# Optimization experiments

Hardware: AMD Instinct MI355X
Metric: run time of the kernel (lower is better)

Reference implementation:

```python
import jax, jax.numpy as jnp
import numpy as np
from jax import lax

B, L, D, H, OM = 16, 512, 2048, 512, 5


def _lstm(seq, wih, whh, bih, bhh):
    # seq: [T, B, F]; PyTorch gate order i, f, g, o
    Hh = whh.shape[1]
    Bb = seq.shape[1]
    def step(carry, xt):
        h, c = carry
        g = xt @ wih.T + h @ whh.T + bih + bhh
        i, f, gg, o = jnp.split(g, 4, axis=-1)
        c = jax.nn.sigmoid(f) * c + jax.nn.sigmoid(i) * jnp.tanh(gg)
        h = jax.nn.sigmoid(o) * jnp.tanh(c)
        return (h, c), h
    z = jnp.zeros((Bb, Hh), seq.dtype)
    _, hs = lax.scan(step, (z, z), seq)
    return hs  # [T, B, Hh]


def setup_inputs() -> dict:
    key = jax.random.key(0)
    ks = jax.random.split(key, 17)
    s = 0.02
    f32 = jnp.float32
    inp = {
        "x": jax.random.normal(ks[0], (B, L, D), f32),
        "wb": jax.random.normal(ks[1], (H, D, OM), f32) * s,
        "bb": jax.random.normal(ks[2], (H,), f32) * s,
        "wa": jax.random.normal(ks[3], (H, D, OM), f32) * s,
        "ba": jax.random.normal(ks[4], (H,), f32) * s,
        "wr": jax.random.normal(ks[5], (H, D, 2 * OM), f32) * s,
        "br": jax.random.normal(ks[6], (H,), f32) * s,
        "wih_f": jax.random.normal(ks[7], (4 * H, H + 1), f32) * s,
        "whh_f": jax.random.normal(ks[8], (4 * H, H), f32) * s,
        "bih_f": jax.random.normal(ks[9], (4 * H,), f32) * s,
        "bhh_f": jax.random.normal(ks[10], (4 * H,), f32) * s,
        "wih_r": jax.random.normal(ks[11], (4 * H, H + 1), f32) * s,
        "whh_r": jax.random.normal(ks[12], (4 * H, H), f32) * s,
        "bih_r": jax.random.normal(ks[13], (4 * H,), f32) * s,
        "bhh_r": jax.random.normal(ks[14], (4 * H,), f32) * s,
        "wfc": jax.random.normal(ks[15], (1, 2 * H), f32) * s,
        "bfc": jax.random.normal(ks[16], (1,), f32) * s,
    }
    return inp


def reference(x, wb, bb, wa, ba, wr, br, wih_f, whh_f, bih_f, bhh_f,
              wih_r, whh_r, bih_r, bhh_r, wfc, bfc):
    om = OM
    xc = jnp.transpose(x, (0, 2, 1))  # [B, D, L]
    conv = lambda w, b: lax.conv_general_dilated(
        xc, w, (1,), 'VALID', dimension_numbers=('NCH', 'OIH', 'NCH')) + b[None, :, None]
    cb = conv(wb, bb)  # [B, H, L-om+1]
    ca = conv(wa, ba)  # [B, H, L-om+1]
    cr = conv(wr, br)  # [B, H, L-2om+1]
    T = x.shape[1] - 2 * om  # number of centers c in [om, L-om)
    d_before = cb[:, :, 0:T]          # window [c-om, c) == conv output c-om
    d_after = ca[:, :, om:om + T]     # window [c, c+om) == conv output c
    vts_d = jnp.sum(d_before * d_after, axis=1, keepdims=True)  # [B, 1, T]
    vts_r = cr[:, :, 0:T]             # full window; pool over length-1 is identity
    vts_seq = jnp.concatenate([vts_r, vts_d], axis=1)  # [B, H+1, T]
    seq = jnp.transpose(vts_seq, (2, 0, 1))  # [T, B, H+1]
    hs_f = _lstm(seq, wih_f, whh_f, bih_f, bhh_f)
    hs_r = _lstm(seq[::-1], wih_r, whh_r, bih_r, bhh_r)[::-1]
    h = jnp.concatenate([hs_f, hs_r], axis=-1)  # [T, B, 2H]
    logits = jnp.einsum('tbh,h->tb', h, wfc[0]) + bfc[0]
    return jax.nn.sigmoid(jnp.transpose(logits))  # [B, T]
```

## Files before the change

### kernel.cpp

```cpp
#include <hip/hip_runtime.h>
#include <hip/hip_bf16.h>

typedef short v8s __attribute__((ext_vector_type(8)));
typedef float v4f __attribute__((ext_vector_type(4)));
typedef unsigned int u32;
typedef unsigned int u32x4 __attribute__((ext_vector_type(4)));
typedef unsigned short u16;
typedef unsigned long long u64;

__device__ __forceinline__ u16 f2bf(float f) {
    union { float f; u32 u; } x; x.f = f;
    u32 r = x.u + 0x7fffu + ((x.u >> 16) & 1u);
    return (u16)(r >> 16);
}
__device__ __forceinline__ float bf2f(u16 s) {
    union { u32 u; float f; } x; x.u = ((u32)s) << 16;
    return x.f;
}
__device__ __forceinline__ float sigmoidf_(float x) { return 1.f / (1.f + __expf(-x)); }
__device__ __forceinline__ float tanh_fast(float x) {
    float t = fminf(fmaxf(x, -15.f), 15.f);
    float e = __expf(2.f * t);
    return (e - 1.f) / (e + 1.f);
}

__global__ __launch_bounds__(256) void xbf_kernel(const float* __restrict__ x, u16* __restrict__ xbf, int n) {
    int i = (blockIdx.x * 256 + threadIdx.x) * 4;
    if (i + 3 < n) {
        float4 v = *(const float4*)(x + i);
        u16* d = xbf + i;
        d[0] = f2bf(v.x); d[1] = f2bf(v.y); d[2] = f2bf(v.z); d[3] = f2bf(v.w);
    }
}

__global__ __launch_bounds__(256) void packw_kernel(const float* __restrict__ wb, const float* __restrict__ wa,
                                                    const float* __restrict__ wr, u16* __restrict__ W1, u16* __restrict__ W2) {
    long e = ((long)blockIdx.x * 256 + threadIdx.x) * 4;
    int which = e >= (1024L * 10240) ? 1 : 0;
    long rem = e - (long)which * 1024 * 10240;
    int n = (int)(rem / 10240);
    int kap = (int)(rem % 10240);
    int tap = kap >> 11, d = kap & 2047;
    u16 o[4];
    if (n < 512) {
        const float* src = which ? wa : wb;
#pragma unroll
        for (int q = 0; q < 4; ++q) o[q] = f2bf(src[(long)n * 10240 + (d + q) * 5 + tap]);
    } else {
        const float* src = wr + (long)(n - 512) * 20480 + tap + (which ? 5 : 0);
#pragma unroll
        for (int q = 0; q < 4; ++q) o[q] = f2bf(src[(d + q) * 10]);
    }
    *(u64*)((which ? W2 : W1) + rem) = *(const u64*)o;
}

__global__ __launch_bounds__(256) void packwih_kernel(const float* __restrict__ wf, const float* __restrict__ wr,
                                                      u16* __restrict__ Bp) {
    int idx = blockIdx.x * 256 + threadIdx.x;
    int n = idx / 576, kap = idx % 576;
    int dir = n >> 11, g = n & 2047;
    const float* src = dir ? wr : wf;
    float v = (kap < 513) ? src[(long)g * 513 + kap] : 0.f;
    Bp[idx] = f2bf(v);
}

__global__ __launch_bounds__(256) void packwhh_kernel(const float* __restrict__ whf, const float* __restrict__ whr,
                                                      u16* __restrict__ W) {
    int idx = blockIdx.x * 256 + threadIdx.x;
    int dir = idx >> 20;
    float v = dir ? whr[idx & 1048575] : whf[idx];
    W[idx] = f2bf(v);
}

__global__ __launch_bounds__(256) void misc_kernel(const float* __restrict__ bihf, const float* __restrict__ bhhf,
                                                   const float* __restrict__ bihr, const float* __restrict__ bhhr,
                                                   float* __restrict__ bsum, u64* __restrict__ hbuf) {
    int i = blockIdx.x * 256 + threadIdx.x;
    if (i < 2048) bsum[i] = bihf[i] + bhhf[i];
    else if (i < 4096) bsum[i] = bihr[i - 2048] + bhhr[i - 2048];
    else if (i < 4096 + 16384) hbuf[i - 4096] = 0xFFFFFFFF00000000ULL;
}

template <int OUTBF>
__global__ __launch_bounds__(256) void gemm_bf16(const u16* __restrict__ A, const u16* __restrict__ B,
                                                 void* __restrict__ Cv, int M, int N, int K, int ldc,
                                                 int row_div, u32 row_mul1, u32 row_mul2, u32 row_base) {
    __shared__ u16 ldsA[128 * 64];
    __shared__ u16 ldsB[128 * 64];
    const int ntn = N >> 7;
    const int nwg = gridDim.x;
    const int bid = blockIdx.x;
    const int swz = (bid & 7) * (nwg >> 3) + (bid >> 3);
    const int tm = swz / ntn, tn = swz % ntn;
    const int tid = threadIdx.x, lane = tid & 63, wv = tid >> 6;
    const int wm = wv >> 1, wn = wv & 1;
    const int qbase = wv * 4;

    u32 asrc[4], bsrc[4];
#pragma unroll
    for (int it = 0; it < 4; ++it) {
        int q = qbase + it;
        int r = q * 8 + (lane >> 3);
        int cb = ((lane & 7) * 16) ^ ((r & 7) << 4);
        int m = tm * 128 + r; if (m > M - 1) m = M - 1;
        asrc[it] = row_base + (u32)(m / row_div) * row_mul1 + (u32)(m % row_div) * row_mul2 + (u32)(cb >> 1);
        int n = tn * 128 + r;
        bsrc[it] = (u32)n * (u32)K + (u32)(cb >> 1);
    }

    v4f acc[4][4];
#pragma unroll
    for (int i = 0; i < 4; ++i)
#pragma unroll
        for (int j = 0; j < 4; ++j) acc[i][j] = (v4f){0.f, 0.f, 0.f, 0.f};

    const int KT = K >> 6;
    for (int kt = 0; kt < KT; ++kt) {
        const int k0 = kt << 6;
#pragma unroll
        for (int it = 0; it < 4; ++it) {
            int q = qbase + it;
            __builtin_amdgcn_global_load_lds(
                (const __attribute__((address_space(1))) u32*)(A + asrc[it] + k0),
                (__attribute__((address_space(3))) u32*)((char*)ldsA + q * 1024), 16, 0, 0);
            __builtin_amdgcn_global_load_lds(
                (const __attribute__((address_space(1))) u32*)(B + bsrc[it] + k0),
                (__attribute__((address_space(3))) u32*)((char*)ldsB + q * 1024), 16, 0, 0);
        }
        __syncthreads();
#pragma unroll
        for (int kk = 0; kk < 2; ++kk) {
            v8s af[4], bfr[4];
#pragma unroll
            for (int i = 0; i < 4; ++i) {
                int row = wm * 64 + i * 16 + (lane & 15);
                int cbyte = (kk * 64 + ((lane >> 4) * 16)) ^ ((row & 7) << 4);
                af[i] = *(const v8s*)((const char*)ldsA + row * 128 + cbyte);
                int rn = wn * 64 + i * 16 + (lane & 15);
                int cbn = (kk * 64 + ((lane >> 4) * 16)) ^ ((rn & 7) << 4);
                bfr[i] = *(const v8s*)((const char*)ldsB + rn * 128 + cbn);
            }
#pragma unroll
            for (int i = 0; i < 4; ++i)
#pragma unroll
                for (int j = 0; j < 4; ++j)
                    acc[i][j] = __builtin_amdgcn_mfma_f32_16x16x32_bf16(af[i], bfr[j], acc[i][j], 0, 0, 0);
        }
        __syncthreads();
    }
#pragma unroll
    for (int i = 0; i < 4; ++i)
#pragma unroll
        for (int j = 0; j < 4; ++j)
#pragma unroll
            for (int r = 0; r < 4; ++r) {
                int m = tm * 128 + wm * 64 + i * 16 + (lane >> 4) * 4 + r;
                int n = tn * 128 + wn * 64 + j * 16 + (lane & 15);
                if (m < M) {
                    if (OUTBF) ((u16*)Cv)[(long)m * ldc + n] = f2bf(acc[i][j][r]);
                    else       ((float*)Cv)[(long)m * ldc + n] = acc[i][j][r];
                }
            }
}

__global__ __launch_bounds__(256) void combine_kernel(const float* __restrict__ G1, const float* __restrict__ G2,
                                                      const float* __restrict__ bb, const float* __restrict__ ba,
                                                      const float* __restrict__ br, u16* __restrict__ seqpad) {
    int m = blockIdx.x;
    int b = m / 502, t = m % 502;
    int tid = threadIdx.x;
    const float* g1 = G1 + (long)m * 1024;
    const float* g2 = G2 + (long)m * 1024;
    u16* dst = seqpad + (long)(t * 16 + b) * 576;
    float part = 0.f;
#pragma unroll
    for (int rep = 0; rep < 2; ++rep) {
        int u = tid + rep * 256;
        float db = g1[u] + bb[u];
        float da = g2[u] + ba[u];
        part += db * da;
        float vr = g1[512 + u] + g2[512 + u] + br[u];
        dst[u] = f2bf(vr);
    }
#pragma unroll
    for (int off = 32; off; off >>= 1) part += __shfl_down(part, off, 64);
    __shared__ float red[4];
    if ((tid & 63) == 0) red[tid >> 6] = part;
    __syncthreads();
    if (tid == 0) dst[512] = f2bf(red[0] + red[1] + red[2] + red[3]);
    if (tid >= 1 && tid < 64) dst[512 + tid] = 0;
}

__global__ __launch_bounds__(256, 1) void lstm_kernel(const u16* __restrict__ P, const u16* __restrict__ whhbf,
                                                      const float* __restrict__ bsum, u64* hbuf,
                                                      u16* __restrict__ hs) {
    const int wg = blockIdx.x;
    const int dir = wg >> 4, j = wg & 15;
    const int tid = threadIdx.x, lane = tid & 63, w = tid >> 6;
    __shared__ u16 hls[16 * 512];
    __shared__ float gls[4][16][32];

    v8s bf[2][16];
    const u16* whd = whhbf + (long)dir * 2048 * 512;
#pragma unroll
    for (int nt = 0; nt < 2; ++nt) {
        int n = w * 512 + j * 32 + nt * 16 + (lane & 15);
#pragma unroll
        for (int kt = 0; kt < 16; ++kt)
            bf[nt][kt] = *(const v8s*)(whd + (long)n * 512 + kt * 32 + ((lane >> 4) * 8));
    }

    for (int i = tid; i < 8192; i += 256) hls[i] = 0;

    const int b_ = tid >> 4;
    const int u_ = (tid * 2) & 31;
    float c0 = 0.f, c1 = 0.f;
    u64* hb = hbuf + dir * 2 * 4096;
    const int col0 = w * 512 + j * 32 + (lane & 15);
    const float bs0 = bsum[dir * 2048 + col0];
    const float bs1 = bsum[dir * 2048 + col0 + 16];
    const u16* Pd = P + dir * 2048;

    float pv[2][4];
    {
        int tau = dir ? 501 : 0;
#pragma unroll
        for (int nt = 0; nt < 2; ++nt)
#pragma unroll
            for (int r = 0; r < 4; ++r)
                pv[nt][r] = bf2f(Pd[(long)(tau * 16 + ((lane >> 4) * 4 + r)) * 4096 + col0 + nt * 16]);
    }
    __syncthreads();

    for (int s = 0; s < 502; ++s) {
        const int tau = dir ? (501 - s) : s;
        if (s > 0) {
            const u64* slotp = hb + ((s - 1) & 1) * 4096;
            const u32 want = (u32)(s - 1);
            u64 base = (u64)slotp + (u64)tid * 16;
            u64 a0 = base,          a1 = base + 4096,  a2 = base + 8192,  a3 = base + 12288;
            u64 a4 = base + 16384,  a5 = base + 20480, a6 = base + 24576, a7 = base + 28672;
            u32x4 w0, w1, w2, w3, w4, w5, w6, w7;
            for (;;) {
                asm volatile(
                    "global_load_dwordx4 %[w0], %[a0], off sc1\n\t"
                    "global_load_dwordx4 %[w1], %[a1], off sc1\n\t"
                    "global_load_dwordx4 %[w2], %[a2], off sc1\n\t"
                    "global_load_dwordx4 %[w3], %[a3], off sc1\n\t"
                    "global_load_dwordx4 %[w4], %[a4], off sc1\n\t"
                    "global_load_dwordx4 %[w5], %[a5], off sc1\n\t"
                    "global_load_dwordx4 %[w6], %[a6], off sc1\n\t"
                    "global_load_dwordx4 %[w7], %[a7], off sc1\n\t"
                    "s_waitcnt vmcnt(0)"
                    : [w0]"=v"(w0), [w1]"=v"(w1), [w2]"=v"(w2), [w3]"=v"(w3),
                      [w4]"=v"(w4), [w5]"=v"(w5), [w6]"=v"(w6), [w7]"=v"(w7)
                    : [a0]"v"(a0), [a1]"v"(a1), [a2]"v"(a2), [a3]"v"(a3),
                      [a4]"v"(a4), [a5]"v"(a5), [a6]"v"(a6), [a7]"v"(a7)
                    : "memory");
                u32 ok = (w0[1] == want) + (w0[3] == want) + (w1[1] == want) + (w1[3] == want)
                       + (w2[1] == want) + (w2[3] == want) + (w3[1] == want) + (w3[3] == want)
                       + (w4[1] == want) + (w4[3] == want) + (w5[1] == want) + (w5[3] == want)
                       + (w6[1] == want) + (w6[3] == want) + (w7[1] == want) + (w7[3] == want);
                if (ok == 16) break;
            }
#define FILL(rep, pay0, pay1) {                                                             \
            int i0 = tid * 2 + (rep) * 512;                                                 \
            int bb2 = i0 >> 8; int p = i0 & 255;                                            \
            int bo = (bb2 << 10) + ((p << 2) ^ ((bb2 & 7) << 4));                           \
            *(u32*)((char*)hls + bo) = (pay0);                                              \
            int i1 = i0 + 1; int p1 = i1 & 255;                                             \
            int bo1 = (bb2 << 10) + ((p1 << 2) ^ ((bb2 & 7) << 4));                         \
            *(u32*)((char*)hls + bo1) = (pay1); }
            FILL(0, w0[0], w0[2]) FILL(1, w1[0], w1[2]) FILL(2, w2[0], w2[2]) FILL(3, w3[0], w3[2])
            FILL(4, w4[0], w4[2]) FILL(5, w5[0], w5[2]) FILL(6, w6[0], w6[2]) FILL(7, w7[0], w7[2])
#undef FILL
        }
        __syncthreads();
        v4f a0a, a1a, a0b = (v4f){0, 0, 0, 0}, a1b = (v4f){0, 0, 0, 0};
#pragma unroll
        for (int r = 0; r < 4; ++r) { a0a[r] = pv[0][r] + bs0; a1a[r] = pv[1][r] + bs1; }
#pragma unroll
        for (int kt = 0; kt < 16; kt += 2) {
            int row = lane & 15;
            int cb0 = (kt * 64 + ((lane >> 4) * 16)) ^ ((row & 7) << 4);
            int cb1 = ((kt + 1) * 64 + ((lane >> 4) * 16)) ^ ((row & 7) << 4);
            v8s af0 = *(const v8s*)((const char*)hls + row * 1024 + cb0);
            v8s af1 = *(const v8s*)((const char*)hls + row * 1024 + cb1);
            a0a = __builtin_amdgcn_mfma_f32_16x16x32_bf16(af0, bf[0][kt], a0a, 0, 0, 0);
            a1a = __builtin_amdgcn_mfma_f32_16x16x32_bf16(af0, bf[1][kt], a1a, 0, 0, 0);
            a0b = __builtin_amdgcn_mfma_f32_16x16x32_bf16(af1, bf[0][kt + 1], a0b, 0, 0, 0);
            a1b = __builtin_amdgcn_mfma_f32_16x16x32_bf16(af1, bf[1][kt + 1], a1b, 0, 0, 0);
        }
#pragma unroll
        for (int r = 0; r < 4; ++r) {
            gls[w][(lane >> 4) * 4 + r][(lane & 15)] = a0a[r] + a0b[r];
            gls[w][(lane >> 4) * 4 + r][16 + (lane & 15)] = a1a[r] + a1b[r];
        }
        __syncthreads();
        float i0 = gls[0][b_][u_],     f0 = gls[1][b_][u_],     g0 = gls[2][b_][u_],     o0 = gls[3][b_][u_];
        float i1 = gls[0][b_][u_ + 1], f1 = gls[1][b_][u_ + 1], g1v = gls[2][b_][u_ + 1], o1 = gls[3][b_][u_ + 1];
        c0 = sigmoidf_(f0) * c0 + sigmoidf_(i0) * tanh_fast(g0);
        c1 = sigmoidf_(f1) * c1 + sigmoidf_(i1) * tanh_fast(g1v);
        float h0 = sigmoidf_(o0) * tanh_fast(c0);
        float h1 = sigmoidf_(o1) * tanh_fast(c1);
        u32 hw = (u32)f2bf(h0) | ((u32)f2bf(h1) << 16);
        int gi = (b_ * 512 + j * 32 + u_) >> 1;
        __hip_atomic_store(hb + (s & 1) * 4096 + gi, (u64)hw | ((u64)(u32)s << 32),
                           __ATOMIC_RELAXED, __HIP_MEMORY_SCOPE_AGENT);
        *(u32*)(hs + (((long)(dir * 502 + tau) * 16 + b_) * 512 + j * 32 + u_)) = hw;
        if (s + 1 < 502) {
            int tau2 = dir ? (500 - s) : (s + 1);
#pragma unroll
            for (int nt = 0; nt < 2; ++nt)
#pragma unroll
                for (int r = 0; r < 4; ++r)
                    pv[nt][r] = bf2f(Pd[(long)(tau2 * 16 + ((lane >> 4) * 4 + r)) * 4096 + col0 + nt * 16]);
        }
    }
}

__global__ __launch_bounds__(256) void final_kernel(const u16* __restrict__ hs, const float* __restrict__ wfc,
                                                    const float* __restrict__ bfc, float* __restrict__ out) {
    int m = blockIdx.x;
    int t = m >> 4, b = m & 15;
    int tid = threadIdx.x;
    const u16* hf = hs + ((long)t * 16 + b) * 512;
    const u16* hr = hs + ((long)(502 + t) * 16 + b) * 512;
    float part = 0.f;
#pragma unroll
    for (int rep = 0; rep < 2; ++rep) {
        int u = tid + rep * 256;
        part += bf2f(hf[u]) * wfc[u] + bf2f(hr[u]) * wfc[512 + u];
    }
#pragma unroll
    for (int off = 32; off; off >>= 1) part += __shfl_down(part, off, 64);
    __shared__ float red[4];
    if ((tid & 63) == 0) red[tid >> 6] = part;
    __syncthreads();
    if (tid == 0) {
        float lg = red[0] + red[1] + red[2] + red[3] + bfc[0];
        out[(long)b * 502 + t] = 1.f / (1.f + __expf(-lg));
    }
}

extern "C" void kernel_launch(void* const* d_in, const int* in_sizes, int n_in,
                              void* d_out, int out_size, void* d_ws, size_t ws_size,
                              hipStream_t stream) {
    const float* x     = (const float*)d_in[0];
    const float* wb    = (const float*)d_in[1];
    const float* bb    = (const float*)d_in[2];
    const float* wa    = (const float*)d_in[3];
    const float* ba    = (const float*)d_in[4];
    const float* wr    = (const float*)d_in[5];
    const float* br    = (const float*)d_in[6];
    const float* wih_f = (const float*)d_in[7];
    const float* whh_f = (const float*)d_in[8];
    const float* bih_f = (const float*)d_in[9];
    const float* bhh_f = (const float*)d_in[10];
    const float* wih_r = (const float*)d_in[11];
    const float* whh_r = (const float*)d_in[12];
    const float* bih_r = (const float*)d_in[13];
    const float* bhh_r = (const float*)d_in[14];
    const float* wfc   = (const float*)d_in[15];
    const float* bfc   = (const float*)d_in[16];
    float* out = (float*)d_out;

    char* ws = (char*)d_ws;
    u16* xbf = (u16*)ws;
    u16* W1  = (u16*)(ws + 33554432);
    u16* W2  = (u16*)(ws + 54525952);
    u16* Pb  = (u16*)ws;
    char* r2 = ws + 75497472;
    float* G1 = (float*)r2;
    float* G2 = (float*)(r2 + 32899072);
    u16*  hs  = (u16*)r2;
    char* r3 = r2 + 65798144;
    u16*  seqp = (u16*)r3;
    u16*  wihp = (u16*)(r3 + 9252864);
    u16*  whhb = (u16*)(r3 + 13971456);
    float* bsum= (float*)(r3 + 18165760);
    u64*  hbuf = (u64*)(r3 + 18182144);

    xbf_kernel<<<16384, 256, 0, stream>>>(x, xbf, 16 * 512 * 2048);
    packw_kernel<<<20480, 256, 0, stream>>>(wb, wa, wr, W1, W2);
    packwih_kernel<<<9216, 256, 0, stream>>>(wih_f, wih_r, wihp);
    packwhh_kernel<<<8192, 256, 0, stream>>>(whh_f, whh_r, whhb);
    misc_kernel<<<80, 256, 0, stream>>>(bih_f, bhh_f, bih_r, bhh_r, bsum, hbuf);

    gemm_bf16<0><<<63 * 8, 256, 0, stream>>>(xbf, W1, G1, 8032, 1024, 10240, 1024,
                                             502, 512u * 2048u, 2048u, 0u);
    gemm_bf16<0><<<63 * 8, 256, 0, stream>>>(xbf, W2, G2, 8032, 1024, 10240, 1024,
                                             502, 512u * 2048u, 2048u, 5u * 2048u);
    combine_kernel<<<8032, 256, 0, stream>>>(G1, G2, bb, ba, br, seqp);
    gemm_bf16<1><<<63 * 32, 256, 0, stream>>>(seqp, wihp, Pb, 8032, 4096, 576, 4096,
                                              8032, 0u, 576u, 0u);
    lstm_kernel<<<32, 256, 0, stream>>>(Pb, whhb, bsum, hbuf, hs);
    final_kernel<<<8032, 256, 0, stream>>>(hs, wfc, bfc, out);
}
```

Baseline: 1.741 ms.

## Halve LSTM workgroups to 8 per direction with 512 threads each

The recurrent LSTM kernel now runs 8 workgroups of 8 waves per direction instead of 16 workgroups of 4 waves, with each workgroup owning 64 hidden units. Each wave still holds the same slice of Whh in registers. Fewer workgroups take part in the per-timestep global flag exchange, and each thread polls 4 instead of 8 vectors, which aims to cut the cross-workgroup synchronization latency on every step. The cost is more intra-workgroup barrier work over 8 waves and only 16 CUs in use.

```diff
diff --git a/kernel.cpp b/kernel.cpp
--- a/kernel.cpp
+++ b/kernel.cpp
@@ -191,32 +191,34 @@
     if (tid >= 1 && tid < 64) dst[512 + tid] = 0;
 }
 
-__global__ __launch_bounds__(256, 1) void lstm_kernel(const u16* __restrict__ P, const u16* __restrict__ whhbf,
+__global__ __launch_bounds__(512, 1) void lstm_kernel(const u16* __restrict__ P, const u16* __restrict__ whhbf,
                                                       const float* __restrict__ bsum, u64* hbuf,
                                                       u16* __restrict__ hs) {
     const int wg = blockIdx.x;
-    const int dir = wg >> 4, j = wg & 15;
+    const int dir = wg >> 3, j = wg & 7;
     const int tid = threadIdx.x, lane = tid & 63, w = tid >> 6;
+    const int g = w & 3, half = w >> 2;
     __shared__ u16 hls[16 * 512];
-    __shared__ float gls[4][16][32];
+    __shared__ float gls[4][16][64];
 
     v8s bf[2][16];
     const u16* whd = whhbf + (long)dir * 2048 * 512;
 #pragma unroll
     for (int nt = 0; nt < 2; ++nt) {
-        int n = w * 512 + j * 32 + nt * 16 + (lane & 15);
+        int n = g * 512 + j * 64 + half * 32 + nt * 16 + (lane & 15);
 #pragma unroll
         for (int kt = 0; kt < 16; ++kt)
             bf[nt][kt] = *(const v8s*)(whd + (long)n * 512 + kt * 32 + ((lane >> 4) * 8));
     }
 
-    for (int i = tid; i < 8192; i += 256) hls[i] = 0;
-
-    const int b_ = tid >> 4;
-    const int u_ = (tid * 2) & 31;
+    for (int i = tid; i < 8192; i += 512) hls[i] = 0;
+
+    const int b_ = tid >> 5;
+    const int p_ = tid & 31;
+    const int u_ = p_ * 2;
     float c0 = 0.f, c1 = 0.f;
     u64* hb = hbuf + dir * 2 * 4096;
-    const int col0 = w * 512 + j * 32 + (lane & 15);
+    const int col0 = g * 512 + j * 64 + half * 32 + (lane & 15);
     const float bs0 = bsum[dir * 2048 + col0];
     const float bs1 = bsum[dir * 2048 + col0 + 16];
     const u16* Pd = P + dir * 2048;
@@ -238,41 +240,31 @@
             const u64* slotp = hb + ((s - 1) & 1) * 4096;
             const u32 want = (u32)(s - 1);
             u64 base = (u64)slotp + (u64)tid * 16;
-            u64 a0 = base,          a1 = base + 4096,  a2 = base + 8192,  a3 = base + 12288;
-            u64 a4 = base + 16384,  a5 = base + 20480, a6 = base + 24576, a7 = base + 28672;
-            u32x4 w0, w1, w2, w3, w4, w5, w6, w7;
+            u64 a0 = base, a1 = base + 8192, a2 = base + 16384, a3 = base + 24576;
+            u32x4 w0, w1, w2, w3;
             for (;;) {
                 asm volatile(
                     "global_load_dwordx4 %[w0], %[a0], off sc1\n\t"
                     "global_load_dwordx4 %[w1], %[a1], off sc1\n\t"
                     "global_load_dwordx4 %[w2], %[a2], off sc1\n\t"
                     "global_load_dwordx4 %[w3], %[a3], off sc1\n\t"
-                    "global_load_dwordx4 %[w4], %[a4], off sc1\n\t"
-                    "global_load_dwordx4 %[w5], %[a5], off sc1\n\t"
-                    "global_load_dwordx4 %[w6], %[a6], off sc1\n\t"
-                    "global_load_dwordx4 %[w7], %[a7], off sc1\n\t"
                     "s_waitcnt vmcnt(0)"
-                    : [w0]"=v"(w0), [w1]"=v"(w1), [w2]"=v"(w2), [w3]"=v"(w3),
-                      [w4]"=v"(w4), [w5]"=v"(w5), [w6]"=v"(w6), [w7]"=v"(w7)
-                    : [a0]"v"(a0), [a1]"v"(a1), [a2]"v"(a2), [a3]"v"(a3),
-                      [a4]"v"(a4), [a5]"v"(a5), [a6]"v"(a6), [a7]"v"(a7)
+                    : [w0]"=v"(w0), [w1]"=v"(w1), [w2]"=v"(w2), [w3]"=v"(w3)
+                    : [a0]"v"(a0), [a1]"v"(a1), [a2]"v"(a2), [a3]"v"(a3)
                     : "memory");
                 u32 ok = (w0[1] == want) + (w0[3] == want) + (w1[1] == want) + (w1[3] == want)
-                       + (w2[1] == want) + (w2[3] == want) + (w3[1] == want) + (w3[3] == want)
-                       + (w4[1] == want) + (w4[3] == want) + (w5[1] == want) + (w5[3] == want)
-                       + (w6[1] == want) + (w6[3] == want) + (w7[1] == want) + (w7[3] == want);
-                if (ok == 16) break;
+                       + (w2[1] == want) + (w2[3] == want) + (w3[1] == want) + (w3[3] == want);
+                if (ok == 8) break;
             }
 #define FILL(rep, pay0, pay1) {                                                             \
-            int i0 = tid * 2 + (rep) * 512;                                                 \
+            int i0 = tid * 2 + (rep) * 1024;                                                \
             int bb2 = i0 >> 8; int p = i0 & 255;                                            \
             int bo = (bb2 << 10) + ((p << 2) ^ ((bb2 & 7) << 4));                           \
             *(u32*)((char*)hls + bo) = (pay0);                                              \
-            int i1 = i0 + 1; int p1 = i1 & 255;                                             \
+            int p1 = p + 1;                                                                 \
             int bo1 = (bb2 << 10) + ((p1 << 2) ^ ((bb2 & 7) << 4));                         \
             *(u32*)((char*)hls + bo1) = (pay1); }
             FILL(0, w0[0], w0[2]) FILL(1, w1[0], w1[2]) FILL(2, w2[0], w2[2]) FILL(3, w3[0], w3[2])
-            FILL(4, w4[0], w4[2]) FILL(5, w5[0], w5[2]) FILL(6, w6[0], w6[2]) FILL(7, w7[0], w7[2])
 #undef FILL
         }
         __syncthreads();
@@ -293,8 +285,9 @@
         }
 #pragma unroll
         for (int r = 0; r < 4; ++r) {
-            gls[w][(lane >> 4) * 4 + r][(lane & 15)] = a0a[r] + a0b[r];
-            gls[w][(lane >> 4) * 4 + r][16 + (lane & 15)] = a1a[r] + a1b[r];
+            int rr = (lane >> 4) * 4 + r;
+            gls[g][rr][half * 32 + (lane & 15)] = a0a[r] + a0b[r];
+            gls[g][rr][half * 32 + 16 + (lane & 15)] = a1a[r] + a1b[r];
         }
         __syncthreads();
         float i0 = gls[0][b_][u_],     f0 = gls[1][b_][u_],     g0 = gls[2][b_][u_],     o0 = gls[3][b_][u_];
@@ -304,10 +297,10 @@
         float h0 = sigmoidf_(o0) * tanh_fast(c0);
         float h1 = sigmoidf_(o1) * tanh_fast(c1);
         u32 hw = (u32)f2bf(h0) | ((u32)f2bf(h1) << 16);
-        int gi = (b_ * 512 + j * 32 + u_) >> 1;
-        __hip_atomic_store(hb + (s & 1) * 4096 + gi, (u64)hw | ((u64)(u32)s << 32),
+        __hip_atomic_store(hb + (s & 1) * 4096 + b_ * 256 + j * 32 + p_,
+                           (u64)hw | ((u64)(u32)s << 32),
                            __ATOMIC_RELAXED, __HIP_MEMORY_SCOPE_AGENT);
-        *(u32*)(hs + (((long)(dir * 502 + tau) * 16 + b_) * 512 + j * 32 + u_)) = hw;
+        *(u32*)(hs + (((long)(dir * 502 + tau) * 16 + b_) * 512 + j * 64 + u_)) = hw;
         if (s + 1 < 502) {
             int tau2 = dir ? (500 - s) : (s + 1);
 #pragma unroll
@@ -394,6 +387,6 @@
     combine_kernel<<<8032, 256, 0, stream>>>(G1, G2, bb, ba, br, seqp);
     gemm_bf16<1><<<63 * 32, 256, 0, stream>>>(seqp, wihp, Pb, 8032, 4096, 576, 4096,
                                               8032, 0u, 576u, 0u);
-    lstm_kernel<<<32, 256, 0, stream>>>(Pb, whhb, bsum, hbuf, hs);
+    lstm_kernel<<<16, 512, 0, stream>>>(Pb, whhb, bsum, hbuf, hs);
     final_kernel<<<8032, 256, 0, stream>>>(hs, wfc, bfc, out);
 }
```

Measured after the change: 1.890 ms. +8.5%, slower.

## Add dedicated conv GEMM with 256x128 tiles and 4-stage direct-to-LDS pipeline

Applied to the files above, without the earlier changes.

Replaces the generic bf16 GEMM for the two large conv GEMMs with a specialized kernel using 512-thread blocks, 256x128 output tiles, and global_load_lds direct-to-LDS loads with a 4-stage ring buffer and raised wave priority around MFMA. This targets global-to-LDS latency and register staging overhead on the dominant compute stage. It uses 96KB LDS and one block per CU, with 256 blocks per launch, which may leave some CUs idle or underfill. A small index simplification in the LSTM fill macro is also included.

```diff
diff --git a/kernel.cpp b/kernel.cpp
--- a/kernel.cpp
+++ b/kernel.cpp
@@ -79,6 +79,107 @@
     if (i < 2048) bsum[i] = bihf[i] + bhhf[i];
     else if (i < 4096) bsum[i] = bihr[i - 2048] + bhhr[i - 2048];
     else if (i < 4096 + 16384) hbuf[i - 4096] = 0xFFFFFFFF00000000ULL;
+}
+
+__global__ __launch_bounds__(512, 1) void gemm_conv(const u16* __restrict__ A, const u16* __restrict__ B,
+                                                    float* __restrict__ C, u32 row_base) {
+    const int M = 8032, K = 10240, NT = 320;
+    __shared__ char lds[98304];
+    const int tn = blockIdx.x & 7;
+    const int tm = blockIdx.x >> 3;
+    const int tid = threadIdx.x, lane = tid & 63, w = tid >> 6;
+    const int wm = w >> 1, wn = w & 1;
+    const int lane15 = lane & 15, kgrp = lane >> 4;
+
+    u32 asrc[2], bsrc;
+#pragma unroll
+    for (int r = 0; r < 2; ++r) {
+        int l = r * 8192 + tid * 16;
+        int rp = l >> 7, inner = l & 127;
+        int innp = inner ^ ((rp & 7) << 4);
+        int row = rp * 2 + (innp >> 6);
+        int kb = innp & 63;
+        int m = tm * 256 + row; if (m > M - 1) m = M - 1;
+        asrc[r] = row_base + (u32)(m / 502) * (512u * 2048u) + (u32)(m % 502) * 2048u + (u32)(kb >> 1);
+    }
+    {
+        int l = tid * 16;
+        int rp = l >> 7, inner = l & 127;
+        int innp = inner ^ ((rp & 7) << 4);
+        int row = rp * 2 + (innp >> 6);
+        int kb = innp & 63;
+        bsrc = (u32)(tn * 128 + row) * (u32)K + (u32)(kb >> 1);
+    }
+    int aoff[4], boff[4];
+#pragma unroll
+    for (int i = 0; i < 4; ++i) {
+        int row = wm * 64 + i * 16 + lane15;
+        int rp = row >> 1;
+        aoff[i] = rp * 128 + ((((row & 1) << 6) | (kgrp * 16)) ^ ((rp & 7) << 4));
+        int rowb = wn * 64 + i * 16 + lane15;
+        int rpb = rowb >> 1;
+        boff[i] = rpb * 128 + ((((rowb & 1) << 6) | (kgrp * 16)) ^ ((rpb & 7) << 4));
+    }
+
+    v4f acc[4][4];
+#pragma unroll
+    for (int i = 0; i < 4; ++i)
+#pragma unroll
+        for (int j = 0; j < 4; ++j) acc[i][j] = (v4f){0.f, 0.f, 0.f, 0.f};
+
+#define ISSUE(t) {                                                                          \
+        int s_ = (t) & 3;                                                                   \
+        __builtin_amdgcn_global_load_lds(                                                   \
+            (const __attribute__((address_space(1))) u32*)(A + asrc[0] + (t) * 32),         \
+            (__attribute__((address_space(3))) u32*)(lds + s_ * 16384 + w * 1024), 16, 0, 0);\
+        __builtin_amdgcn_global_load_lds(                                                   \
+            (const __attribute__((address_space(1))) u32*)(A + asrc[1] + (t) * 32),         \
+            (__attribute__((address_space(3))) u32*)(lds + s_ * 16384 + 8192 + w * 1024), 16, 0, 0);\
+        __builtin_amdgcn_global_load_lds(                                                   \
+            (const __attribute__((address_space(1))) u32*)(B + bsrc + (t) * 32),            \
+            (__attribute__((address_space(3))) u32*)(lds + 65536 + s_ * 8192 + w * 1024), 16, 0, 0);\
+    }
+
+    ISSUE(0) ISSUE(1) ISSUE(2)
+    asm volatile("s_waitcnt vmcnt(6)" ::: "memory");
+    __builtin_amdgcn_s_barrier();
+    asm volatile("" ::: "memory");
+
+    for (int kt = 0; kt < NT; ++kt) {
+        const char* As = lds + (kt & 3) * 16384;
+        const char* Bs = lds + 65536 + (kt & 3) * 8192;
+        v8s a[4], b[4];
+#pragma unroll
+        for (int i = 0; i < 4; ++i) {
+            a[i] = *(const v8s*)(As + aoff[i]);
+            b[i] = *(const v8s*)(Bs + boff[i]);
+        }
+        if (kt + 3 < NT) ISSUE(kt + 3)
+        __builtin_amdgcn_s_setprio(1);
+#pragma unroll
+        for (int i = 0; i < 4; ++i)
+#pragma unroll
+            for (int j = 0; j < 4; ++j)
+                acc[i][j] = __builtin_amdgcn_mfma_f32_16x16x32_bf16(a[i], b[j], acc[i][j], 0, 0, 0);
+        __builtin_amdgcn_s_setprio(0);
+        if (kt + 3 < NT)      { asm volatile("s_waitcnt vmcnt(6)" ::: "memory"); }
+        else if (kt + 2 < NT) { asm volatile("s_waitcnt vmcnt(3)" ::: "memory"); }
+        else                  { asm volatile("s_waitcnt vmcnt(0)" ::: "memory"); }
+        __builtin_amdgcn_s_barrier();
+        asm volatile("" ::: "memory");
+    }
+#undef ISSUE
+
+#pragma unroll
+    for (int i = 0; i < 4; ++i)
+#pragma unroll
+        for (int j = 0; j < 4; ++j)
+#pragma unroll
+            for (int r = 0; r < 4; ++r) {
+                int m = tm * 256 + wm * 64 + i * 16 + kgrp * 4 + r;
+                int n = tn * 128 + wn * 64 + j * 16 + lane15;
+                if (m < M) C[(long)m * 1024 + n] = acc[i][j][r];
+            }
 }
 
 template <int OUTBF>
@@ -268,7 +369,7 @@
             int bb2 = i0 >> 8; int p = i0 & 255;                                            \
             int bo = (bb2 << 10) + ((p << 2) ^ ((bb2 & 7) << 4));                           \
             *(u32*)((char*)hls + bo) = (pay0);                                              \
-            int i1 = i0 + 1; int p1 = i1 & 255;                                             \
+            int p1 = p + 1;                                                                 \
             int bo1 = (bb2 << 10) + ((p1 << 2) ^ ((bb2 & 7) << 4));                         \
             *(u32*)((char*)hls + bo1) = (pay1); }
             FILL(0, w0[0], w0[2]) FILL(1, w1[0], w1[2]) FILL(2, w2[0], w2[2]) FILL(3, w3[0], w3[2])
@@ -387,10 +488,8 @@
     packwhh_kernel<<<8192, 256, 0, stream>>>(whh_f, whh_r, whhb);
     misc_kernel<<<80, 256, 0, stream>>>(bih_f, bhh_f, bih_r, bhh_r, bsum, hbuf);
 
-    gemm_bf16<0><<<63 * 8, 256, 0, stream>>>(xbf, W1, G1, 8032, 1024, 10240, 1024,
-                                             502, 512u * 2048u, 2048u, 0u);
-    gemm_bf16<0><<<63 * 8, 256, 0, stream>>>(xbf, W2, G2, 8032, 1024, 10240, 1024,
-                                             502, 512u * 2048u, 2048u, 5u * 2048u);
+    gemm_conv<<<256, 512, 0, stream>>>(xbf, W1, G1, 0u);
+    gemm_conv<<<256, 512, 0, stream>>>(xbf, W2, G2, 5u * 2048u);
     combine_kernel<<<8032, 256, 0, stream>>>(G1, G2, bb, ba, br, seqp);
     gemm_bf16<1><<<63 * 32, 256, 0, stream>>>(seqp, wihp, Pb, 8032, 4096, 576, 4096,
                                               8032, 0u, 576u, 0u);
```

Result: faster. 1.677 ms (-3.7%).
